# Optimization experiments

Measured on AMD Instinct MI355X. Metric: run time of the kernel, lower is better.

The kernel has to match this reference:

```python
import jax, jax.numpy as jnp
import numpy as np

B, N, T, FB, HID, NC = 1024, 64, 256, 5, 64, 3
T2 = T // 2
EPS = 1e-5


def setup_inputs() -> dict:
    key = jax.random.key(0)
    ks = jax.random.split(key, 40)
    it = iter(range(40))
    def nrm(shape, s=0.1):
        return (jax.random.normal(ks[next(it)], shape, dtype=jnp.float32) * s)
    inp = {}
    inp["x_T"] = jax.random.normal(ks[next(it)], (B, N, T), dtype=jnp.float32)
    inp["x_F"] = jax.random.normal(ks[next(it)], (B, N, FB), dtype=jnp.float32)
    inp["A"] = jax.random.uniform(ks[next(it)], (B, N, N), dtype=jnp.float32)
    # STDCN_F (seq len = FB, input=hidden=N)
    inp["gcnw_F"] = jnp.full((1, 1), 10.0, dtype=jnp.float32)
    for d in ("f", "b"):
        inp[f"gru_F_wih_{d}"] = nrm((3 * N, N))
        inp[f"gru_F_whh_{d}"] = nrm((3 * N, N))
        inp[f"gru_F_bih_{d}"] = nrm((3 * N,))
        inp[f"gru_F_bhh_{d}"] = nrm((3 * N,))
    inp["bn_F_g"] = jnp.ones((FB,), jnp.float32)
    inp["bn_F_b"] = jnp.zeros((FB,), jnp.float32)
    # STDCN_T (seq len = T)
    inp["gcnw_T"] = jnp.full((1, 1), 10.0, dtype=jnp.float32)
    for d in ("f", "b"):
        inp[f"gru_T_wih_{d}"] = nrm((3 * N, N))
        inp[f"gru_T_whh_{d}"] = nrm((3 * N, N))
        inp[f"gru_T_bih_{d}"] = nrm((3 * N,))
        inp[f"gru_T_bhh_{d}"] = nrm((3 * N,))
    inp["bn_T_g"] = jnp.ones((T,), jnp.float32)
    inp["bn_T_b"] = jnp.zeros((T,), jnp.float32)
    # heads
    inp["linF_w"] = nrm((T2, FB))
    inp["linF_b"] = nrm((T2,))
    inp["linT_w"] = nrm((T2, T), 0.05)
    inp["linT_b"] = nrm((T2,))
    inp["lin1_w"] = nrm((HID, T * N * 2), 0.01)
    inp["lin1_b"] = nrm((HID,))
    inp["lin2_w"] = nrm((NC, HID))
    inp["lin2_b"] = nrm((NC,))
    return inp


def _leaky(x):
    return jnp.where(x >= 0, x, 0.01 * x)


def _norm_adj(A):
    # zero diagonal, add self loops, symmetric D^-1/2 A D^-1/2
    I = jnp.eye(A.shape[1], dtype=A.dtype)
    H = A * (1.0 - I) + I
    dinv = jnp.sum(H, axis=-1) ** -0.5  # [B,N]
    return dinv[:, :, None] * H * dinv[:, None, :]


def _gru_dir(x, wih, whh, bih, bhh):
    # x: [B,S,N] -> outputs [B,S,Nh]; torch GRU cell equations
    gx = jnp.einsum("bsn,gn->bsg", x, wih) + bih  # [B,S,3Nh]
    gx = jnp.swapaxes(gx, 0, 1)  # [S,B,3Nh]
    Nh = whh.shape[1]
    h0 = jnp.zeros((x.shape[0], Nh), x.dtype)
    def step(h, g):
        gh = h @ whh.T + bhh
        xr, xz, xn = jnp.split(g, 3, axis=-1)
        hr, hz, hn = jnp.split(gh, 3, axis=-1)
        r = jax.nn.sigmoid(xr + hr)
        z = jax.nn.sigmoid(xz + hz)
        n = jnp.tanh(xn + r * hn)
        h = (1.0 - z) * n + z * h
        return h, h
    _, hs = jax.lax.scan(step, h0, gx)
    return jnp.swapaxes(hs, 0, 1)


def _gru_bi(x, pf, pb):
    f = _gru_dir(x, *pf)
    b = _gru_dir(x[:, ::-1], *pb)[:, ::-1]
    return jnp.concatenate([f, b], axis=-1)


def _batchnorm(x, g, b):
    # x: [B, F, C]; BatchNorm1d over channel dim 1, training-mode batch stats
    m = jnp.mean(x, axis=(0, 2), keepdims=True)
    v = jnp.var(x, axis=(0, 2), keepdims=True)
    return g[None, :, None] * (x - m) / jnp.sqrt(v + EPS) + b[None, :, None]


def _stdcn(X, Hn, w, pf, pb, g, bparam):
    # gcn_conv loop == (H @ X) * scalar weight
    Xc = _leaky(jnp.einsum("bij,bjf->bif", Hn, X) * w[0, 0])
    Xp = jnp.swapaxes(Xc, 1, 2)  # [B,F,N]
    o = _gru_bi(Xp, pf, pb)      # [B,F,2N]
    o = _batchnorm(o, g, bparam)
    return jnp.swapaxes(o, 1, 2)  # [B,2N,F]


def reference(x_T, x_F, A, gcnw_F, gru_F_wih_f, gru_F_whh_f, gru_F_bih_f, gru_F_bhh_f,
              gru_F_wih_b, gru_F_whh_b, gru_F_bih_b, gru_F_bhh_b, bn_F_g, bn_F_b,
              gcnw_T, gru_T_wih_f, gru_T_whh_f, gru_T_bih_f, gru_T_bhh_f,
              gru_T_wih_b, gru_T_whh_b, gru_T_bih_b, gru_T_bhh_b, bn_T_g, bn_T_b,
              linF_w, linF_b, linT_w, linT_b, lin1_w, lin1_b, lin2_w, lin2_b):
    Hn = _norm_adj(A)
    out_F = _stdcn(x_F, Hn, gcnw_F,
                   (gru_F_wih_f, gru_F_whh_f, gru_F_bih_f, gru_F_bhh_f),
                   (gru_F_wih_b, gru_F_whh_b, gru_F_bih_b, gru_F_bhh_b),
                   bn_F_g, bn_F_b)  # [B,2N,FB]
    out_F = (out_F @ linF_w.T + linF_b).reshape(out_F.shape[0], -1)  # [B, 2N*T2]
    out_T = _stdcn(x_T, Hn, gcnw_T,
                   (gru_T_wih_f, gru_T_whh_f, gru_T_bih_f, gru_T_bhh_f),
                   (gru_T_wih_b, gru_T_whh_b, gru_T_bih_b, gru_T_bhh_b),
                   bn_T_g, bn_T_b)  # [B,2N,T]
    out_T = (out_T @ linT_w.T + linT_b).reshape(out_T.shape[0], -1)
    out = jnp.concatenate([out_F, out_T], axis=-1)  # [B, 2*N*T]
    out = _leaky(out @ lin1_w.T + lin1_b)
    return out @ lin2_w.T + lin2_b  # [B, NC]
```

## Files before the change

kernel.cpp:

```cpp
#include <hip/hip_runtime.h>

#define B_ 1024
#define N_ 64
#define T_ 256
#define FB_ 5
#define T2_ 128
#define C_ 128

typedef unsigned short u16;
typedef __attribute__((ext_vector_type(8))) short bf16x8;
typedef __attribute__((ext_vector_type(4))) float f32x4;

__device__ __forceinline__ float leaky(float x) { return x >= 0.f ? x : 0.01f * x; }
__device__ __forceinline__ float rcpf(float x) { return __builtin_amdgcn_rcpf(x); }
__device__ __forceinline__ float sigm2(float x) { return rcpf(1.f + __expf(-x)); }
__device__ __forceinline__ float tanh2(float x) { return 1.f - 2.f * rcpf(1.f + __expf(2.f * x)); }
__device__ __forceinline__ unsigned bf16_rne(float f) {
  unsigned u = __float_as_uint(f);
  return (u + 0x7FFFu + ((u >> 16) & 1u)) >> 16;
}
__device__ __forceinline__ void block_sync_lds() {
  __builtin_amdgcn_sched_barrier(0);
  asm volatile("s_waitcnt lgkmcnt(0)" ::: "memory");
  __builtin_amdgcn_s_barrier();
  __builtin_amdgcn_sched_barrier(0);
}

#define MFMA_(A, B, C) __builtin_amdgcn_mfma_f32_16x16x32_bf16(A, B, C, 0, 0, 0)

__device__ __forceinline__ void xc_tile(const float (*HsT)[68], float (*xs)[68],
                                        const float* __restrict__ Xb, int S, int t0, float w,
                                        float* __restrict__ Ob, int tid) {
  __syncthreads();
  for (int idx = tid; idx < 4096; idx += 256) {
    int j = idx >> 6, tt = idx & 63;
    xs[j][tt] = (t0 + tt < S) ? Xb[j * S + t0 + tt] : 0.f;
  }
  __syncthreads();
  int i0 = (tid & 15) * 4, tl = (tid >> 4) * 4;
  f32x4 a0 = {0, 0, 0, 0}, a1 = {0, 0, 0, 0}, a2 = {0, 0, 0, 0}, a3 = {0, 0, 0, 0};
#pragma unroll 4
  for (int j = 0; j < 64; ++j) {
    f32x4 hv = *(const f32x4*)&HsT[j][i0];
    f32x4 xv = *(const f32x4*)&xs[j][tl];
    a0 += hv * xv[0];
    a1 += hv * xv[1];
    a2 += hv * xv[2];
    a3 += hv * xv[3];
  }
#define STORE_T(K, AV)                                  \
  {                                                     \
    int t = t0 + tl + K;                                \
    if (t < S) {                                        \
      f32x4 r;                                          \
      _Pragma("unroll") for (int e = 0; e < 4; ++e)     \
          r[e] = leaky(w * AV[e]);                      \
      *(f32x4*)&Ob[(size_t)t * 64 + i0] = r;            \
    }                                                   \
  }
  STORE_T(0, a0)
  STORE_T(1, a1)
  STORE_T(2, a2)
  STORE_T(3, a3)
#undef STORE_T
}

__global__ __launch_bounds__(256) void knorm_xc(
    const float* __restrict__ A, const float* __restrict__ xT, const float* __restrict__ xF,
    const float* __restrict__ wT, const float* __restrict__ wF,
    float* __restrict__ XpT, float* __restrict__ XpF) {
  __shared__ float HsT[64][68];
  __shared__ float dinv[64];
  __shared__ float xs[64][68];
  int b = blockIdx.x, tid = threadIdx.x;
  const float* Ab = A + (size_t)b * 4096;
  for (int idx = tid; idx < 4096; idx += 256) {
    int i = idx >> 6, j = idx & 63;
    HsT[j][i] = (i == j) ? 1.f : Ab[idx];
  }
  __syncthreads();
  if (tid < 64) {
    float s = 0.f;
    for (int j = 0; j < 64; ++j) s += HsT[j][tid];
    dinv[tid] = 1.f / sqrtf(s);
  }
  __syncthreads();
  for (int idx = tid; idx < 4096; idx += 256) {
    int j = idx >> 6, i = idx & 63;
    HsT[j][i] *= dinv[i] * dinv[j];
  }
  {
    const float* Xb = xT + (size_t)b * 64 * 256;
    float w = wT[0];
    float* Ob = XpT + (size_t)b * 256 * 64;
    for (int t0 = 0; t0 < 256; t0 += 64) xc_tile(HsT, xs, Xb, 256, t0, w, Ob, tid);
  }
  {
    const float* Xb = xF + (size_t)b * 64 * 5;
    float w = wF[0];
    float* Ob = XpF + (size_t)b * 5 * 64;
    xc_tile(HsT, xs, Xb, 5, 0, w, Ob, tid);
  }
}

__global__ __launch_bounds__(256) void kxq_all(const float* __restrict__ XpT,
                                               const float* __restrict__ XpF,
                                               u16* __restrict__ XfT, u16* __restrict__ XfF) {
  __shared__ float xs[4][16][68];
  int bt = blockIdx.x, by = blockIdx.y, tid = threadIdx.x;
  const float* Xp;
  u16* Xf;
  int S, t0;
  if (by < 64) {
    Xp = XpT; Xf = XfT; S = 256; t0 = by * 4;
  } else {
    Xp = XpF; Xf = XfF; S = 5; t0 = (by - 64) * 4;
  }
  for (int idx = tid; idx < 1024; idx += 256) {
    int b_l = idx >> 6, rest = idx & 63, t_l = rest >> 4, c = rest & 15;
    float4 v = {0.f, 0.f, 0.f, 0.f};
    if (t0 + t_l < S)
      v = *(const float4*)(Xp + ((size_t)(bt * 16 + b_l) * S + t0 + t_l) * 64 + c * 4);
    *(float4*)&xs[t_l][b_l][c * 4] = v;
  }
  __syncthreads();
  int t_l = tid >> 6, lane = tid & 63, blo = lane & 15, grp = lane >> 4;
  int t = t0 + t_l;
  if (t >= S) return;
#pragma unroll
  for (int kh = 0; kh < 2; ++kh) {
    const f32x4* src = (const f32x4*)&xs[t_l][blo][kh * 32 + grp * 8];
    f32x4 a0 = src[0], a1 = src[1];
    bf16x8 hi, lo;
#pragma unroll
    for (int e = 0; e < 4; ++e) {
      unsigned h0 = bf16_rne(a0[e]);
      hi[e] = (short)h0;
      lo[e] = (short)bf16_rne(a0[e] - __uint_as_float(h0 << 16));
      unsigned h1 = bf16_rne(a1[e]);
      hi[e + 4] = (short)h1;
      lo[e + 4] = (short)bf16_rne(a1[e] - __uint_as_float(h1 << 16));
    }
    u16* dst = Xf + (size_t)(bt * S + t) * 2048 + (size_t)kh * 1024 + lane * 8;
    *(bf16x8*)dst = hi;
    *(bf16x8*)(dst + 512) = lo;
  }
}

__device__ __forceinline__ void axcomp(f32x4 (&AX)[3], const bf16x8 (&XB)[4],
                                       const bf16x8 (&Whi)[3][2], const bf16x8 (&Wlo)[3][2],
                                       const f32x4 (&bI)[3]) {
  AX[0] = bI[0];
  AX[1] = bI[1];
  AX[2] = bI[2];
#pragma unroll
  for (int kh = 0; kh < 2; ++kh) {
    bf16x8 xh = XB[2 * kh], xl = XB[2 * kh + 1];
#pragma unroll
    for (int gi = 0; gi < 3; ++gi) {
      AX[gi] = MFMA_(Whi[gi][kh], xh, AX[gi]);
      AX[gi] = MFMA_(Whi[gi][kh], xl, AX[gi]);
      AX[gi] = MFMA_(Wlo[gi][kh], xh, AX[gi]);
    }
  }
}

__global__ __launch_bounds__(256, 1) void kgru_all(
    const u16* __restrict__ XfT, const u16* __restrict__ XfF,
    const float* __restrict__ Twih_f, const float* __restrict__ Twhh_f,
    const float* __restrict__ Tbih_f, const float* __restrict__ Tbhh_f,
    const float* __restrict__ Twih_b, const float* __restrict__ Twhh_b,
    const float* __restrict__ Tbih_b, const float* __restrict__ Tbhh_b,
    const float* __restrict__ Fwih_f, const float* __restrict__ Fwhh_f,
    const float* __restrict__ Fbih_f, const float* __restrict__ Fbhh_f,
    const float* __restrict__ Fwih_b, const float* __restrict__ Fwhh_b,
    const float* __restrict__ Fbih_b, const float* __restrict__ Fbhh_b,
    u16* __restrict__ gT, u16* __restrict__ gF,
    const float* __restrict__ W1, const float* __restrict__ lTw, const float* __restrict__ lFw,
    const float* __restrict__ lFb, const float* __restrict__ lTb, const float* __restrict__ l1b,
    float* __restrict__ MT, float* __restrict__ MF, float* __restrict__ c0v) {
  __shared__ u16 Hhi[2][16][72];
  __shared__ u16 Hlo[2][16][72];
  __shared__ float W1s[128][129];
  __shared__ float ls[128][32];
  __shared__ float rs[256];
  int tid = threadIdx.x;
  int w = tid >> 6, lane = tid & 63, blo = lane & 15, grp = lane >> 4;
  int bt = blockIdx.x, dir = blockIdx.y, tf = blockIdx.z;
  int S = tf ? 5 : 256;
  const u16* Xf = tf ? XfF : XfT;
  u16* g = tf ? gF : gT;
  const float* wih = tf ? (dir ? Fwih_b : Fwih_f) : (dir ? Twih_b : Twih_f);
  const float* whh = tf ? (dir ? Fwhh_b : Fwhh_f) : (dir ? Twhh_b : Twhh_f);
  const float* bih = tf ? (dir ? Fbih_b : Fbih_f) : (dir ? Tbih_b : Tbih_f);
  const float* bhh = tf ? (dir ? Fbhh_b : Fbhh_f) : (dir ? Tbhh_b : Tbhh_f);

  for (int idx = tid; idx < 16 * 72; idx += 256) {
    ((u16*)Hhi[0])[idx] = 0;
    ((u16*)Hlo[0])[idx] = 0;
  }

  bf16x8 Wih_hi[3][2], Wih_lo[3][2], Whh_hi[3][2], Whh_lo[3][2];
#pragma unroll
  for (int gi = 0; gi < 3; ++gi) {
    int k = (gi * 4 + w) * 16 + blo;
#pragma unroll
    for (int kh = 0; kh < 2; ++kh) {
      int j0 = kh * 32 + grp * 8;
#pragma unroll
      for (int m = 0; m < 2; ++m) {
        const float* src = (m ? whh : wih) + (size_t)k * 64 + j0;
        f32x4 a0 = *(const f32x4*)src;
        f32x4 a1 = *(const f32x4*)(src + 4);
        bf16x8 hi, lo;
#pragma unroll
        for (int e = 0; e < 4; ++e) {
          unsigned h0 = bf16_rne(a0[e]);
          hi[e] = (short)h0;
          lo[e] = (short)bf16_rne(a0[e] - __uint_as_float(h0 << 16));
          unsigned h1 = bf16_rne(a1[e]);
          hi[e + 4] = (short)h1;
          lo[e + 4] = (short)bf16_rne(a1[e] - __uint_as_float(h1 << 16));
        }
        if (m) {
          Whh_hi[gi][kh] = hi;
          Whh_lo[gi][kh] = lo;
        } else {
          Wih_hi[gi][kh] = hi;
          Wih_lo[gi][kh] = lo;
        }
      }
    }
  }
  f32x4 bI[3], bH[3];
#pragma unroll
  for (int gi = 0; gi < 3; ++gi) {
    int k0 = (gi * 4 + w) * 16 + 4 * grp;
    bI[gi] = *(const f32x4*)(bih + k0);
    bH[gi] = *(const f32x4*)(bhh + k0);
  }

  float ho[4] = {0.f, 0.f, 0.f, 0.f};
  int j0q = 16 * w + 4 * grp;
  const u16* xbase = Xf + (size_t)bt * S * 2048 + lane * 8;
  long long sstep = dir ? -4096LL : 4096LL;
  long long gstep = dir ? -256LL : 256LL;

  bf16x8 x0[4], x1[4], x2[4], x3[4];
#define LOADX(DST, TR)                            \
  {                                               \
    const u16* xp = xbase + (size_t)(TR) * 2048;  \
    DST[0] = *(const bf16x8*)(xp);                \
    DST[1] = *(const bf16x8*)(xp + 512);          \
    DST[2] = *(const bf16x8*)(xp + 1024);         \
    DST[3] = *(const bf16x8*)(xp + 1536);         \
  }
  LOADX(x0, dir ? (S - 1) : 0)
  if (S > 1) LOADX(x1, dir ? (S - 2) : 1)
  if (S > 2) LOADX(x2, dir ? (S - 3) : 2)
  const u16* xw = xbase + (size_t)(dir ? (S >= 4 ? S - 4 : 0) : 3) * 2048;
  u16* gp = g + ((size_t)(bt * 16 + blo) * S + (dir ? S - 1 : 0)) * 128 + dir * 64 + j0q;

  f32x4 axA[3], axB[3];
  axcomp(axA, x0, Wih_hi, Wih_lo, bI);
  block_sync_lds();

#define GSTEP(KK, XAX, XLD, AXC, AXN, PR, PW)                                        \
  {                                                                                  \
    int t = tbase + KK;                                                              \
    if (t < S) {                                                                     \
      bf16x8 h0h = *(const bf16x8*)&Hhi[PR][blo][grp * 8];                           \
      bf16x8 h0l = *(const bf16x8*)&Hlo[PR][blo][grp * 8];                           \
      bf16x8 h1h = *(const bf16x8*)&Hhi[PR][blo][32 + grp * 8];                      \
      bf16x8 h1l = *(const bf16x8*)&Hlo[PR][blo][32 + grp * 8];                      \
      if (t + 3 < S) {                                                               \
        XLD[0] = *(const bf16x8*)(xw);                                               \
        XLD[1] = *(const bf16x8*)(xw + 512);                                         \
        XLD[2] = *(const bf16x8*)(xw + 1024);                                        \
        XLD[3] = *(const bf16x8*)(xw + 1536);                                        \
        xw = (const u16*)((const char*)xw + sstep);                                  \
      }                                                                              \
      if (t + 1 < S) axcomp(AXN, XAX, Wih_hi, Wih_lo, bI);                           \
      f32x4 ahr = bH[0], ahz = bH[1], ahn = bH[2];                                   \
      ahr = MFMA_(Whh_hi[0][0], h0h, ahr);                                           \
      ahr = MFMA_(Whh_hi[0][0], h0l, ahr);                                           \
      ahr = MFMA_(Whh_lo[0][0], h0h, ahr);                                           \
      ahz = MFMA_(Whh_hi[1][0], h0h, ahz);                                           \
      ahz = MFMA_(Whh_hi[1][0], h0l, ahz);                                           \
      ahz = MFMA_(Whh_lo[1][0], h0h, ahz);                                           \
      ahn = MFMA_(Whh_hi[2][0], h0h, ahn);                                           \
      ahn = MFMA_(Whh_hi[2][0], h0l, ahn);                                           \
      ahn = MFMA_(Whh_lo[2][0], h0h, ahn);                                           \
      ahr = MFMA_(Whh_hi[0][1], h1h, ahr);                                           \
      ahr = MFMA_(Whh_hi[0][1], h1l, ahr);                                           \
      ahr = MFMA_(Whh_lo[0][1], h1h, ahr);                                           \
      ahz = MFMA_(Whh_hi[1][1], h1h, ahz);                                           \
      ahz = MFMA_(Whh_hi[1][1], h1l, ahz);                                           \
      ahz = MFMA_(Whh_lo[1][1], h1h, ahz);                                           \
      ahn = MFMA_(Whh_hi[2][1], h1h, ahn);                                           \
      ahn = MFMA_(Whh_hi[2][1], h1l, ahn);                                           \
      ahn = MFMA_(Whh_lo[2][1], h1h, ahn);                                           \
      u16 hi_u[4], lo_u[4];                                                          \
      _Pragma("unroll") for (int u = 0; u < 4; ++u) {                                \
        float r = sigm2(AXC[0][u] + ahr[u]);                                         \
        float z = sigm2(AXC[1][u] + ahz[u]);                                         \
        float n = tanh2(AXC[2][u] + r * ahn[u]);                                     \
        float h = n + z * (ho[u] - n);                                               \
        ho[u] = h;                                                                   \
        unsigned hb = (__float_as_uint(h) + 0x8000u) >> 16;                          \
        hi_u[u] = (u16)hb;                                                           \
        float rr = h - __uint_as_float(hb << 16);                                    \
        lo_u[u] = (u16)((__float_as_uint(rr) + 0x8000u) >> 16);                      \
      }                                                                              \
      ushort4 h4;                                                                    \
      h4.x = hi_u[0]; h4.y = hi_u[1]; h4.z = hi_u[2]; h4.w = hi_u[3];                \
      ushort4 l4;                                                                    \
      l4.x = lo_u[0]; l4.y = lo_u[1]; l4.z = lo_u[2]; l4.w = lo_u[3];                \
      *(ushort4*)&Hhi[PW][blo][j0q] = h4;                                            \
      *(ushort4*)&Hlo[PW][blo][j0q] = l4;                                            \
      *(ushort4*)gp = h4;                                                            \
      gp = (u16*)((char*)gp + gstep);                                                \
      block_sync_lds();                                                              \
    }                                                                                \
  }

  for (int tbase = 0; tbase < S; tbase += 4) {
    GSTEP(0, x1, x3, axA, axB, 0, 1)
    GSTEP(1, x2, x0, axB, axA, 1, 0)
    GSTEP(2, x3, x1, axA, axB, 0, 1)
    GSTEP(3, x0, x2, axB, axA, 1, 0)
  }
#undef GSTEP
#undef LOADX

  if (tf == 1) {
    int jid = bt * 2 + dir;
    for (int job = jid; job < 576; job += 128) {
      __syncthreads();
      int o = job & 63, by = job >> 6;
      if (by < 8) {
        int t0 = by * 32;
        const float* Wo = W1 + (size_t)o * 32768 + 16384;
        for (int idx = tid; idx < 16384; idx += 256) W1s[idx >> 7][idx & 127] = Wo[idx];
        for (int idx = tid; idx < 4096; idx += 256)
          ls[idx >> 5][idx & 31] = lTw[(idx >> 5) * 256 + t0 + (idx & 31)];
        __syncthreads();
        int c = tid & 127, th = tid >> 7;
        float acc[16];
#pragma unroll
        for (int q = 0; q < 16; ++q) acc[q] = 0.f;
        for (int t2 = 0; t2 < 128; ++t2) {
          float wv = W1s[c][t2];
#pragma unroll
          for (int q = 0; q < 16; ++q) acc[q] += wv * ls[t2][th + 2 * q];
        }
        float* Mo = MT + (size_t)o * 32768;
#pragma unroll
        for (int q = 0; q < 16; ++q) Mo[(t0 + th + 2 * q) * 128 + c] = acc[q];
      } else {
        const float* Wo = W1 + (size_t)o * 32768;
        for (int idx = tid; idx < 16384; idx += 256) W1s[idx >> 7][idx & 127] = Wo[idx];
        for (int idx = tid; idx < 640; idx += 256) ls[idx / 5][idx % 5] = lFw[idx];
        __syncthreads();
        int c = tid & 127, fh = tid >> 7;
        float acc[3] = {0.f, 0.f, 0.f};
        for (int t2 = 0; t2 < 128; ++t2) {
          float wv = W1s[c][t2];
#pragma unroll
          for (int q = 0; q < 3; ++q) {
            int f = fh + 2 * q;
            if (f < 5) acc[q] += wv * ls[t2][f];
          }
        }
#pragma unroll
        for (int q = 0; q < 3; ++q) {
          int f = fh + 2 * q;
          if (f < 5) MF[(size_t)o * 640 + f * 128 + c] = acc[q];
        }
        float s = 0.f;
        for (int idx = tid; idx < 16384; idx += 256) {
          int t2 = idx & 127;
          s += Wo[idx] * lFb[t2] + Wo[16384 + idx] * lTb[t2];
        }
        rs[tid] = s;
        __syncthreads();
        for (int off = 128; off; off >>= 1) {
          if (tid < off) rs[tid] += rs[tid + off];
          __syncthreads();
        }
        if (tid == 0) c0v[o] = l1b[o] + rs[0];
      }
    }
  }
}

__global__ __launch_bounds__(256) void kbn_all(
    const u16* __restrict__ gTp, const u16* __restrict__ gFp,
    const float* __restrict__ gamT, const float* __restrict__ betT,
    const float* __restrict__ gamF, const float* __restrict__ betF,
    float* __restrict__ sdT, float* __restrict__ sdF) {
  int bid = blockIdx.x, tid = threadIdx.x;
  const u16* g;
  const float *gam, *bet;
  float* sd;
  int S, t;
  if (bid < 256) {
    g = gTp; S = 256; t = bid; gam = gamT; bet = betT; sd = sdT;
  } else {
    g = gFp; S = 5; t = bid - 256; gam = gamF; bet = betF; sd = sdF;
  }
  float s = 0.f, s2 = 0.f;
  for (int unit = tid; unit < 32768; unit += 256) {
    int b = unit >> 5, c4 = (unit & 31) * 4;
    ushort4 u = *(const ushort4*)(g + ((size_t)b * S + t) * 128 + c4);
    float v0 = __uint_as_float((unsigned)u.x << 16);
    float v1 = __uint_as_float((unsigned)u.y << 16);
    float v2 = __uint_as_float((unsigned)u.z << 16);
    float v3 = __uint_as_float((unsigned)u.w << 16);
    s += v0 + v1 + v2 + v3;
    s2 += v0 * v0 + v1 * v1 + v2 * v2 + v3 * v3;
  }
  __shared__ float rs[256], rq[256];
  rs[tid] = s;
  rq[tid] = s2;
  __syncthreads();
  for (int off = 128; off; off >>= 1) {
    if (tid < off) {
      rs[tid] += rs[tid + off];
      rq[tid] += rq[tid + off];
    }
    __syncthreads();
  }
  if (tid == 0) {
    float inv_n = 1.f / (float)(B_ * C_);
    float m = rs[0] * inv_n;
    float var = rq[0] * inv_n - m * m;
    float inv = 1.f / sqrtf(var + 1e-5f);
    float sc = gam[t] * inv;
    sd[2 * t] = sc;
    sd[2 * t + 1] = bet[t] - m * sc;
  }
}

__global__ __launch_bounds__(256) void kchunk_all(
    const u16* __restrict__ gTp, const u16* __restrict__ gFp,
    const float* __restrict__ sdT, const float* __restrict__ sdF,
    const float* __restrict__ MT, const float* __restrict__ MF,
    float* __restrict__ part) {
  __shared__ float gs[32][132];
  __shared__ float Ms[64][132];
  int tid = threadIdx.x;
  int b0 = blockIdx.x * 32;
  int by = blockIdx.y;
  const u16* g;
  const float *sd, *M;
  int S, nt, t0, slot;
  if (by < 16) {
    g = gTp; sd = sdT; M = MT; S = 256; nt = 16; t0 = by * 16; slot = by;
  } else {
    g = gFp; sd = sdF; M = MF; S = 5; nt = 5; t0 = 0; slot = 16;
  }
  int ot = tid & 31, bt = tid >> 5;
  float acc[4][2];
#pragma unroll
  for (int i = 0; i < 4; ++i) {
    acc[i][0] = 0.f;
    acc[i][1] = 0.f;
  }
  for (int t = t0; t < t0 + nt; ++t) {
    __syncthreads();
    float sc = sd[2 * t], dd = sd[2 * t + 1];
    for (int idx = tid; idx < 1024; idx += 256) {
      int bb = idx >> 5, c4 = (idx & 31) * 4;
      ushort4 u = *(const ushort4*)(g + ((size_t)(b0 + bb) * S + t) * 128 + c4);
      gs[bb][c4 + 0] = __uint_as_float((unsigned)u.x << 16) * sc + dd;
      gs[bb][c4 + 1] = __uint_as_float((unsigned)u.y << 16) * sc + dd;
      gs[bb][c4 + 2] = __uint_as_float((unsigned)u.z << 16) * sc + dd;
      gs[bb][c4 + 3] = __uint_as_float((unsigned)u.w << 16) * sc + dd;
    }
    for (int idx = tid; idx < 2048; idx += 256) {
      int o = idx >> 5, c4 = (idx & 31) * 4;
      *(float4*)&Ms[o][c4] = *(const float4*)(M + ((size_t)o * S + t) * 128 + c4);
    }
    __syncthreads();
    for (int c = 0; c < 128; c += 4) {
      f32x4 m0 = *(const f32x4*)&Ms[ot][c];
      f32x4 m1 = *(const f32x4*)&Ms[ot + 32][c];
#pragma unroll
      for (int i = 0; i < 4; ++i) {
        f32x4 gv = *(const f32x4*)&gs[bt * 4 + i][c];
        acc[i][0] += gv[0] * m0[0] + gv[1] * m0[1] + gv[2] * m0[2] + gv[3] * m0[3];
        acc[i][1] += gv[0] * m1[0] + gv[1] * m1[1] + gv[2] * m1[2] + gv[3] * m1[3];
      }
    }
  }
#pragma unroll
  for (int i = 0; i < 4; ++i) {
    part[((size_t)slot * 1024 + b0 + bt * 4 + i) * 64 + ot] = acc[i][0];
    part[((size_t)slot * 1024 + b0 + bt * 4 + i) * 64 + ot + 32] = acc[i][1];
  }
}

__global__ __launch_bounds__(64) void kfin(const float* __restrict__ part,
                                           const float* __restrict__ c0,
                                           const float* __restrict__ l2w,
                                           const float* __restrict__ l2b,
                                           float* __restrict__ outp) {
  int b = blockIdx.x, o = threadIdx.x;
  float y = c0[o];
  for (int s = 0; s < 17; ++s) y += part[((size_t)s * 1024 + b) * 64 + o];
  y = leaky(y);
  __shared__ float a[64];
  a[o] = y;
  __syncthreads();
  if (o < 3) {
    float r = l2b[o];
    for (int j = 0; j < 64; ++j) r += l2w[o * 64 + j] * a[j];
    outp[b * 3 + o] = r;
  }
}

extern "C" void kernel_launch(void* const* d_in, const int* in_sizes, int n_in,
                              void* d_out, int out_size, void* d_ws, size_t ws_size,
                              hipStream_t stream) {
  const float* x_T = (const float*)d_in[0];
  const float* x_F = (const float*)d_in[1];
  const float* A = (const float*)d_in[2];
  const float* gcnw_F = (const float*)d_in[3];
  const float* gFwih_f = (const float*)d_in[4];
  const float* gFwhh_f = (const float*)d_in[5];
  const float* gFbih_f = (const float*)d_in[6];
  const float* gFbhh_f = (const float*)d_in[7];
  const float* gFwih_b = (const float*)d_in[8];
  const float* gFwhh_b = (const float*)d_in[9];
  const float* gFbih_b = (const float*)d_in[10];
  const float* gFbhh_b = (const float*)d_in[11];
  const float* bnFg = (const float*)d_in[12];
  const float* bnFb = (const float*)d_in[13];
  const float* gcnw_T = (const float*)d_in[14];
  const float* gTwih_f = (const float*)d_in[15];
  const float* gTwhh_f = (const float*)d_in[16];
  const float* gTbih_f = (const float*)d_in[17];
  const float* gTbhh_f = (const float*)d_in[18];
  const float* gTwih_b = (const float*)d_in[19];
  const float* gTwhh_b = (const float*)d_in[20];
  const float* gTbih_b = (const float*)d_in[21];
  const float* gTbhh_b = (const float*)d_in[22];
  const float* bnTg = (const float*)d_in[23];
  const float* bnTb = (const float*)d_in[24];
  const float* linF_w = (const float*)d_in[25];
  const float* linF_b = (const float*)d_in[26];
  const float* linT_w = (const float*)d_in[27];
  const float* linT_b = (const float*)d_in[28];
  const float* lin1_w = (const float*)d_in[29];
  const float* lin1_b = (const float*)d_in[30];
  const float* lin2_w = (const float*)d_in[31];
  const float* lin2_b = (const float*)d_in[32];

  char* w8 = (char*)d_ws;
  size_t off = 0;
  auto take = [&](size_t bytes) {
    void* p = w8 + off;
    off += (bytes + 255) & ~(size_t)255;
    return p;
  };
  float* XpT = (float*)take((size_t)1024 * 256 * 64 * 4);
  float* XpF = (float*)take((size_t)1024 * 5 * 64 * 4);
  u16* XfT = (u16*)take((size_t)64 * 256 * 2048 * 2);
  u16* XfF = (u16*)take((size_t)64 * 5 * 2048 * 2);
  u16* gT = (u16*)take((size_t)1024 * 256 * 128 * 2);
  u16* gF = (u16*)take((size_t)1024 * 5 * 128 * 2);
  float* sdT = (float*)take(512 * 4);
  float* sdF = (float*)take(16 * 4);
  float* MT = (float*)take((size_t)64 * 256 * 128 * 4);
  float* MF = (float*)take((size_t)64 * 5 * 128 * 4);
  float* c0 = (float*)take(64 * 4);
  float* part = (float*)take((size_t)17 * 1024 * 64 * 4);

  knorm_xc<<<1024, 256, 0, stream>>>(A, x_T, x_F, gcnw_T, gcnw_F, XpT, XpF);
  kxq_all<<<dim3(64, 66), 256, 0, stream>>>(XpT, XpF, XfT, XfF);
  kgru_all<<<dim3(64, 2, 2), 256, 0, stream>>>(
      XfT, XfF, gTwih_f, gTwhh_f, gTbih_f, gTbhh_f, gTwih_b, gTwhh_b, gTbih_b, gTbhh_b,
      gFwih_f, gFwhh_f, gFbih_f, gFbhh_f, gFwih_b, gFwhh_b, gFbih_b, gFbhh_b, gT, gF,
      lin1_w, linT_w, linF_w, linF_b, linT_b, lin1_b, MT, MF, c0);
  kbn_all<<<261, 256, 0, stream>>>(gT, gF, bnTg, bnTb, bnFg, bnFb, sdT, sdF);
  kchunk_all<<<dim3(32, 17), 256, 0, stream>>>(gT, gF, sdT, sdF, MT, MF, part);
  kfin<<<1024, 64, 0, stream>>>(part, c0, lin2_w, lin2_b, (float*)d_out);
}
```

Before: 484.3 us.

## Split GRU hidden-dim reduction across two wave groups with LDS partial sums

Doubles the GRU block to 512 threads and splits the 64-wide K dimension of each gate matmul between two groups of four waves. The second group writes partial gate sums to shared memory, and the first group combines them and applies the nonlinearity. This halves the serial MFMA chain per timestep on the recurrent critical path. In exchange it adds an extra barrier and LDS round-trip per step, and it rescales the epilogue W1-projection work to 512 threads.

```diff
diff --git a/kernel.cpp b/kernel.cpp
--- a/kernel.cpp
+++ b/kernel.cpp
@@ -147,25 +147,21 @@
   }
 }
 
-__device__ __forceinline__ void axcomp(f32x4 (&AX)[3], const bf16x8 (&XB)[4],
-                                       const bf16x8 (&Whi)[3][2], const bf16x8 (&Wlo)[3][2],
-                                       const f32x4 (&bI)[3]) {
-  AX[0] = bI[0];
-  AX[1] = bI[1];
-  AX[2] = bI[2];
-#pragma unroll
-  for (int kh = 0; kh < 2; ++kh) {
-    bf16x8 xh = XB[2 * kh], xl = XB[2 * kh + 1];
-#pragma unroll
-    for (int gi = 0; gi < 3; ++gi) {
-      AX[gi] = MFMA_(Whi[gi][kh], xh, AX[gi]);
-      AX[gi] = MFMA_(Whi[gi][kh], xl, AX[gi]);
-      AX[gi] = MFMA_(Wlo[gi][kh], xh, AX[gi]);
-    }
-  }
-}
-
-__global__ __launch_bounds__(256, 1) void kgru_all(
+__device__ __forceinline__ void axc_h(f32x4 (&AX)[3], const bf16x8 (&XB)[2],
+                                      const bf16x8 (&Whi)[3], const bf16x8 (&Wlo)[3],
+                                      const f32x4 (&bI)[3]) {
+  bf16x8 xh = XB[0], xl = XB[1];
+#pragma unroll
+  for (int gi = 0; gi < 3; ++gi) {
+    f32x4 a = bI[gi];
+    a = MFMA_(Whi[gi], xh, a);
+    a = MFMA_(Whi[gi], xl, a);
+    a = MFMA_(Wlo[gi], xh, a);
+    AX[gi] = a;
+  }
+}
+
+__global__ __launch_bounds__(512, 1) void kgru_all(
     const u16* __restrict__ XfT, const u16* __restrict__ XfF,
     const float* __restrict__ Twih_f, const float* __restrict__ Twhh_f,
     const float* __restrict__ Tbih_f, const float* __restrict__ Tbhh_f,
@@ -181,11 +177,13 @@
     float* __restrict__ MT, float* __restrict__ MF, float* __restrict__ c0v) {
   __shared__ u16 Hhi[2][16][72];
   __shared__ u16 Hlo[2][16][72];
+  __shared__ float PS[4][4][16][20];
   __shared__ float W1s[128][129];
   __shared__ float ls[128][32];
-  __shared__ float rs[256];
+  __shared__ float rs[512];
   int tid = threadIdx.x;
-  int w = tid >> 6, lane = tid & 63, blo = lane & 15, grp = lane >> 4;
+  int wave = tid >> 6, lane = tid & 63, blo = lane & 15, grp = lane >> 4;
+  int w = wave & 3, kh = wave >> 2;
   int bt = blockIdx.x, dir = blockIdx.y, tf = blockIdx.z;
   int S = tf ? 5 : 256;
   const u16* Xf = tf ? XfF : XfT;
@@ -195,65 +193,66 @@
   const float* bih = tf ? (dir ? Fbih_b : Fbih_f) : (dir ? Tbih_b : Tbih_f);
   const float* bhh = tf ? (dir ? Fbhh_b : Fbhh_f) : (dir ? Tbhh_b : Tbhh_f);
 
-  for (int idx = tid; idx < 16 * 72; idx += 256) {
+  for (int idx = tid; idx < 16 * 72; idx += 512) {
     ((u16*)Hhi[0])[idx] = 0;
     ((u16*)Hlo[0])[idx] = 0;
   }
 
-  bf16x8 Wih_hi[3][2], Wih_lo[3][2], Whh_hi[3][2], Whh_lo[3][2];
+  bf16x8 Wih_hi[3], Wih_lo[3], Whh_hi[3], Whh_lo[3];
 #pragma unroll
   for (int gi = 0; gi < 3; ++gi) {
     int k = (gi * 4 + w) * 16 + blo;
-#pragma unroll
-    for (int kh = 0; kh < 2; ++kh) {
-      int j0 = kh * 32 + grp * 8;
-#pragma unroll
-      for (int m = 0; m < 2; ++m) {
-        const float* src = (m ? whh : wih) + (size_t)k * 64 + j0;
-        f32x4 a0 = *(const f32x4*)src;
-        f32x4 a1 = *(const f32x4*)(src + 4);
-        bf16x8 hi, lo;
-#pragma unroll
-        for (int e = 0; e < 4; ++e) {
-          unsigned h0 = bf16_rne(a0[e]);
-          hi[e] = (short)h0;
-          lo[e] = (short)bf16_rne(a0[e] - __uint_as_float(h0 << 16));
-          unsigned h1 = bf16_rne(a1[e]);
-          hi[e + 4] = (short)h1;
-          lo[e + 4] = (short)bf16_rne(a1[e] - __uint_as_float(h1 << 16));
-        }
-        if (m) {
-          Whh_hi[gi][kh] = hi;
-          Whh_lo[gi][kh] = lo;
-        } else {
-          Wih_hi[gi][kh] = hi;
-          Wih_lo[gi][kh] = lo;
-        }
+    int j0 = kh * 32 + grp * 8;
+#pragma unroll
+    for (int m = 0; m < 2; ++m) {
+      const float* src = (m ? whh : wih) + (size_t)k * 64 + j0;
+      f32x4 a0 = *(const f32x4*)src;
+      f32x4 a1 = *(const f32x4*)(src + 4);
+      bf16x8 hi, lo;
+#pragma unroll
+      for (int e = 0; e < 4; ++e) {
+        unsigned h0 = bf16_rne(a0[e]);
+        hi[e] = (short)h0;
+        lo[e] = (short)bf16_rne(a0[e] - __uint_as_float(h0 << 16));
+        unsigned h1 = bf16_rne(a1[e]);
+        hi[e + 4] = (short)h1;
+        lo[e + 4] = (short)bf16_rne(a1[e] - __uint_as_float(h1 << 16));
       }
+      if (m) {
+        Whh_hi[gi] = hi;
+        Whh_lo[gi] = lo;
+      } else {
+        Wih_hi[gi] = hi;
+        Wih_lo[gi] = lo;
+      }
     }
   }
   f32x4 bI[3], bH[3];
 #pragma unroll
   for (int gi = 0; gi < 3; ++gi) {
-    int k0 = (gi * 4 + w) * 16 + 4 * grp;
-    bI[gi] = *(const f32x4*)(bih + k0);
-    bH[gi] = *(const f32x4*)(bhh + k0);
+    if (kh == 0) {
+      int k0 = (gi * 4 + w) * 16 + 4 * grp;
+      bI[gi] = *(const f32x4*)(bih + k0);
+      bH[gi] = *(const f32x4*)(bhh + k0);
+    } else {
+      bI[gi] = (f32x4){0.f, 0.f, 0.f, 0.f};
+      bH[gi] = (f32x4){0.f, 0.f, 0.f, 0.f};
+    }
   }
 
   float ho[4] = {0.f, 0.f, 0.f, 0.f};
   int j0q = 16 * w + 4 * grp;
-  const u16* xbase = Xf + (size_t)bt * S * 2048 + lane * 8;
+  int grp4 = grp * 4, kh32 = kh * 32;
+  const u16* xbase = Xf + (size_t)bt * S * 2048 + (size_t)kh * 1024 + lane * 8;
   long long sstep = dir ? -4096LL : 4096LL;
   long long gstep = dir ? -256LL : 256LL;
 
-  bf16x8 x0[4], x1[4], x2[4], x3[4];
+  bf16x8 x0[2], x1[2], x2[2], x3[2];
 #define LOADX(DST, TR)                            \
   {                                               \
     const u16* xp = xbase + (size_t)(TR) * 2048;  \
     DST[0] = *(const bf16x8*)(xp);                \
     DST[1] = *(const bf16x8*)(xp + 512);          \
-    DST[2] = *(const bf16x8*)(xp + 1024);         \
-    DST[3] = *(const bf16x8*)(xp + 1536);         \
   }
   LOADX(x0, dir ? (S - 1) : 0)
   if (S > 1) LOADX(x1, dir ? (S - 2) : 1)
@@ -262,64 +261,64 @@
   u16* gp = g + ((size_t)(bt * 16 + blo) * S + (dir ? S - 1 : 0)) * 128 + dir * 64 + j0q;
 
   f32x4 axA[3], axB[3];
-  axcomp(axA, x0, Wih_hi, Wih_lo, bI);
+  axc_h(axA, x0, Wih_hi, Wih_lo, bI);
   block_sync_lds();
 
 #define GSTEP(KK, XAX, XLD, AXC, AXN, PR, PW)                                        \
   {                                                                                  \
     int t = tbase + KK;                                                              \
     if (t < S) {                                                                     \
-      bf16x8 h0h = *(const bf16x8*)&Hhi[PR][blo][grp * 8];                           \
-      bf16x8 h0l = *(const bf16x8*)&Hlo[PR][blo][grp * 8];                           \
-      bf16x8 h1h = *(const bf16x8*)&Hhi[PR][blo][32 + grp * 8];                      \
-      bf16x8 h1l = *(const bf16x8*)&Hlo[PR][blo][32 + grp * 8];                      \
+      bf16x8 hh = *(const bf16x8*)&Hhi[PR][blo][kh32 + grp * 8];                     \
+      bf16x8 hl = *(const bf16x8*)&Hlo[PR][blo][kh32 + grp * 8];                     \
       if (t + 3 < S) {                                                               \
         XLD[0] = *(const bf16x8*)(xw);                                               \
         XLD[1] = *(const bf16x8*)(xw + 512);                                         \
-        XLD[2] = *(const bf16x8*)(xw + 1024);                                        \
-        XLD[3] = *(const bf16x8*)(xw + 1536);                                        \
         xw = (const u16*)((const char*)xw + sstep);                                  \
       }                                                                              \
-      if (t + 1 < S) axcomp(AXN, XAX, Wih_hi, Wih_lo, bI);                           \
       f32x4 ahr = bH[0], ahz = bH[1], ahn = bH[2];                                   \
-      ahr = MFMA_(Whh_hi[0][0], h0h, ahr);                                           \
-      ahr = MFMA_(Whh_hi[0][0], h0l, ahr);                                           \
-      ahr = MFMA_(Whh_lo[0][0], h0h, ahr);                                           \
-      ahz = MFMA_(Whh_hi[1][0], h0h, ahz);                                           \
-      ahz = MFMA_(Whh_hi[1][0], h0l, ahz);                                           \
-      ahz = MFMA_(Whh_lo[1][0], h0h, ahz);                                           \
-      ahn = MFMA_(Whh_hi[2][0], h0h, ahn);                                           \
-      ahn = MFMA_(Whh_hi[2][0], h0l, ahn);                                           \
-      ahn = MFMA_(Whh_lo[2][0], h0h, ahn);                                           \
-      ahr = MFMA_(Whh_hi[0][1], h1h, ahr);                                           \
-      ahr = MFMA_(Whh_hi[0][1], h1l, ahr);                                           \
-      ahr = MFMA_(Whh_lo[0][1], h1h, ahr);                                           \
-      ahz = MFMA_(Whh_hi[1][1], h1h, ahz);                                           \
-      ahz = MFMA_(Whh_hi[1][1], h1l, ahz);                                           \
-      ahz = MFMA_(Whh_lo[1][1], h1h, ahz);                                           \
-      ahn = MFMA_(Whh_hi[2][1], h1h, ahn);                                           \
-      ahn = MFMA_(Whh_hi[2][1], h1l, ahn);                                           \
-      ahn = MFMA_(Whh_lo[2][1], h1h, ahn);                                           \
-      u16 hi_u[4], lo_u[4];                                                          \
-      _Pragma("unroll") for (int u = 0; u < 4; ++u) {                                \
-        float r = sigm2(AXC[0][u] + ahr[u]);                                         \
-        float z = sigm2(AXC[1][u] + ahz[u]);                                         \
-        float n = tanh2(AXC[2][u] + r * ahn[u]);                                     \
-        float h = n + z * (ho[u] - n);                                               \
-        ho[u] = h;                                                                   \
-        unsigned hb = (__float_as_uint(h) + 0x8000u) >> 16;                          \
-        hi_u[u] = (u16)hb;                                                           \
-        float rr = h - __uint_as_float(hb << 16);                                    \
-        lo_u[u] = (u16)((__float_as_uint(rr) + 0x8000u) >> 16);                      \
+      ahr = MFMA_(Whh_hi[0], hh, ahr);                                               \
+      ahr = MFMA_(Whh_hi[0], hl, ahr);                                               \
+      ahr = MFMA_(Whh_lo[0], hh, ahr);                                               \
+      ahz = MFMA_(Whh_hi[1], hh, ahz);                                               \
+      ahz = MFMA_(Whh_hi[1], hl, ahz);                                               \
+      ahz = MFMA_(Whh_lo[1], hh, ahz);                                               \
+      ahn = MFMA_(Whh_hi[2], hh, ahn);                                               \
+      ahn = MFMA_(Whh_hi[2], hl, ahn);                                               \
+      ahn = MFMA_(Whh_lo[2], hh, ahn);                                               \
+      if (t + 1 < S) axc_h(AXN, XAX, Wih_hi, Wih_lo, bI);                            \
+      if (kh) {                                                                      \
+        *(f32x4*)&PS[0][w][blo][grp4] = ahr + AXC[0];                                \
+        *(f32x4*)&PS[1][w][blo][grp4] = ahz + AXC[1];                                \
+        *(f32x4*)&PS[2][w][blo][grp4] = ahn;                                         \
+        *(f32x4*)&PS[3][w][blo][grp4] = AXC[2];                                      \
       }                                                                              \
-      ushort4 h4;                                                                    \
-      h4.x = hi_u[0]; h4.y = hi_u[1]; h4.z = hi_u[2]; h4.w = hi_u[3];                \
-      ushort4 l4;                                                                    \
-      l4.x = lo_u[0]; l4.y = lo_u[1]; l4.z = lo_u[2]; l4.w = lo_u[3];                \
-      *(ushort4*)&Hhi[PW][blo][j0q] = h4;                                            \
-      *(ushort4*)&Hlo[PW][blo][j0q] = l4;                                            \
-      *(ushort4*)gp = h4;                                                            \
-      gp = (u16*)((char*)gp + gstep);                                                \
+      block_sync_lds();                                                              \
+      if (!kh) {                                                                     \
+        f32x4 pr = *(const f32x4*)&PS[0][w][blo][grp4];                              \
+        f32x4 pz = *(const f32x4*)&PS[1][w][blo][grp4];                              \
+        f32x4 pan = *(const f32x4*)&PS[2][w][blo][grp4];                             \
+        f32x4 pxn = *(const f32x4*)&PS[3][w][blo][grp4];                             \
+        u16 hi_u[4], lo_u[4];                                                        \
+        _Pragma("unroll") for (int u = 0; u < 4; ++u) {                              \
+          float r = sigm2(AXC[0][u] + ahr[u] + pr[u]);                               \
+          float z = sigm2(AXC[1][u] + ahz[u] + pz[u]);                               \
+          float n = tanh2((AXC[2][u] + pxn[u]) + r * (ahn[u] + pan[u]));             \
+          float h = n + z * (ho[u] - n);                                             \
+          ho[u] = h;                                                                 \
+          unsigned hb = (__float_as_uint(h) + 0x8000u) >> 16;                        \
+          hi_u[u] = (u16)hb;                                                         \
+          float rr = h - __uint_as_float(hb << 16);                                  \
+          lo_u[u] = (u16)((__float_as_uint(rr) + 0x8000u) >> 16);                    \
+        }                                                                            \
+        ushort4 h4;                                                                  \
+        h4.x = hi_u[0]; h4.y = hi_u[1]; h4.z = hi_u[2]; h4.w = hi_u[3];              \
+        ushort4 l4;                                                                  \
+        l4.x = lo_u[0]; l4.y = lo_u[1]; l4.z = lo_u[2]; l4.w = lo_u[3];              \
+        *(ushort4*)&Hhi[PW][blo][j0q] = h4;                                          \
+        *(ushort4*)&Hlo[PW][blo][j0q] = l4;                                          \
+        *(ushort4*)gp = h4;                                                          \
+        gp = (u16*)((char*)gp + gstep);                                              \
+      }                                                                              \
       block_sync_lds();                                                              \
     }                                                                                \
   }
@@ -337,54 +336,54 @@
     int jid = bt * 2 + dir;
     for (int job = jid; job < 576; job += 128) {
       __syncthreads();
-      int o = job & 63, by = job >> 6;
-      if (by < 8) {
-        int t0 = by * 32;
+      int o = job & 63, byy = job >> 6;
+      if (byy < 8) {
+        int t0 = byy * 32;
         const float* Wo = W1 + (size_t)o * 32768 + 16384;
-        for (int idx = tid; idx < 16384; idx += 256) W1s[idx >> 7][idx & 127] = Wo[idx];
-        for (int idx = tid; idx < 4096; idx += 256)
+        for (int idx = tid; idx < 16384; idx += 512) W1s[idx >> 7][idx & 127] = Wo[idx];
+        for (int idx = tid; idx < 4096; idx += 512)
           ls[idx >> 5][idx & 31] = lTw[(idx >> 5) * 256 + t0 + (idx & 31)];
         __syncthreads();
         int c = tid & 127, th = tid >> 7;
-        float acc[16];
-#pragma unroll
-        for (int q = 0; q < 16; ++q) acc[q] = 0.f;
+        float acc[8];
+#pragma unroll
+        for (int q = 0; q < 8; ++q) acc[q] = 0.f;
         for (int t2 = 0; t2 < 128; ++t2) {
           float wv = W1s[c][t2];
 #pragma unroll
-          for (int q = 0; q < 16; ++q) acc[q] += wv * ls[t2][th + 2 * q];
+          for (int q = 0; q < 8; ++q) acc[q] += wv * ls[t2][th + 4 * q];
         }
         float* Mo = MT + (size_t)o * 32768;
 #pragma unroll
-        for (int q = 0; q < 16; ++q) Mo[(t0 + th + 2 * q) * 128 + c] = acc[q];
+        for (int q = 0; q < 8; ++q) Mo[(t0 + th + 4 * q) * 128 + c] = acc[q];
       } else {
         const float* Wo = W1 + (size_t)o * 32768;
-        for (int idx = tid; idx < 16384; idx += 256) W1s[idx >> 7][idx & 127] = Wo[idx];
-        for (int idx = tid; idx < 640; idx += 256) ls[idx / 5][idx % 5] = lFw[idx];
+        for (int idx = tid; idx < 16384; idx += 512) W1s[idx >> 7][idx & 127] = Wo[idx];
+        for (int idx = tid; idx < 640; idx += 512) ls[idx / 5][idx % 5] = lFw[idx];
         __syncthreads();
         int c = tid & 127, fh = tid >> 7;
-        float acc[3] = {0.f, 0.f, 0.f};
+        float acc[2] = {0.f, 0.f};
         for (int t2 = 0; t2 < 128; ++t2) {
           float wv = W1s[c][t2];
 #pragma unroll
-          for (int q = 0; q < 3; ++q) {
-            int f = fh + 2 * q;
+          for (int q = 0; q < 2; ++q) {
+            int f = fh + 4 * q;
             if (f < 5) acc[q] += wv * ls[t2][f];
           }
         }
 #pragma unroll
-        for (int q = 0; q < 3; ++q) {
-          int f = fh + 2 * q;
+        for (int q = 0; q < 2; ++q) {
+          int f = fh + 4 * q;
           if (f < 5) MF[(size_t)o * 640 + f * 128 + c] = acc[q];
         }
         float s = 0.f;
-        for (int idx = tid; idx < 16384; idx += 256) {
+        for (int idx = tid; idx < 16384; idx += 512) {
           int t2 = idx & 127;
           s += Wo[idx] * lFb[t2] + Wo[16384 + idx] * lTb[t2];
         }
         rs[tid] = s;
         __syncthreads();
-        for (int off = 128; off; off >>= 1) {
+        for (int off = 256; off; off >>= 1) {
           if (tid < off) rs[tid] += rs[tid + off];
           __syncthreads();
         }
@@ -579,7 +578,7 @@
 
   knorm_xc<<<1024, 256, 0, stream>>>(A, x_T, x_F, gcnw_T, gcnw_F, XpT, XpF);
   kxq_all<<<dim3(64, 66), 256, 0, stream>>>(XpT, XpF, XfT, XfF);
-  kgru_all<<<dim3(64, 2, 2), 256, 0, stream>>>(
+  kgru_all<<<dim3(64, 2, 2), 512, 0, stream>>>(
       XfT, XfF, gTwih_f, gTwhh_f, gTbih_f, gTbhh_f, gTwih_b, gTwhh_b, gTbih_b, gTbhh_b,
       gFwih_f, gFwhh_f, gFbih_f, gFbhh_f, gFwih_b, gFwhh_b, gFbih_b, gFbhh_b, gT, gF,
       lin1_w, linT_w, linF_w, linF_b, linT_b, lin1_b, MT, MF, c0);
```

After: 495.9 us. 1.02x slower.

## Fuse bf16 hi/lo split into graph-conv kernel and relayout GRU input

Applied to the files above, without the earlier changes.

The graph-convolution kernel now stages its leaky-activated output in shared memory and writes the bf16 hi/lo split directly to the GRU input buffer, removing the separate quantisation kernel and the fp32 intermediate round trip through global memory. The GRU input layout changes to a per-batch contiguous 128-element block (hi and lo interleaved by k-half), so the GRU loads use small offsets within one row instead of strides of 512 elements. This cuts one launch and about 67 MB of global traffic, at the cost of an extra shared buffer and barrier per tile in the fused kernel.

```diff
diff --git a/kernel.cpp b/kernel.cpp
--- a/kernel.cpp
+++ b/kernel.cpp
@@ -28,9 +28,9 @@
 
 #define MFMA_(A, B, C) __builtin_amdgcn_mfma_f32_16x16x32_bf16(A, B, C, 0, 0, 0)
 
-__device__ __forceinline__ void xc_tile(const float (*HsT)[68], float (*xs)[68],
+__device__ __forceinline__ void xc_tile(const float (*HsT)[68], float (*xs)[68], float (*ys)[68],
                                         const float* __restrict__ Xb, int S, int t0, float w,
-                                        float* __restrict__ Ob, int tid) {
+                                        u16* __restrict__ Xft, int tid) {
   __syncthreads();
   for (int idx = tid; idx < 4096; idx += 256) {
     int j = idx >> 6, tt = idx & 63;
@@ -48,31 +48,54 @@
     a2 += hv * xv[2];
     a3 += hv * xv[3];
   }
-#define STORE_T(K, AV)                                  \
+#define YS_T(K, AV)                                     \
   {                                                     \
-    int t = t0 + tl + K;                                \
-    if (t < S) {                                        \
-      f32x4 r;                                          \
-      _Pragma("unroll") for (int e = 0; e < 4; ++e)     \
-          r[e] = leaky(w * AV[e]);                      \
-      *(f32x4*)&Ob[(size_t)t * 64 + i0] = r;            \
-    }                                                   \
-  }
-  STORE_T(0, a0)
-  STORE_T(1, a1)
-  STORE_T(2, a2)
-  STORE_T(3, a3)
-#undef STORE_T
+    f32x4 r;                                            \
+    _Pragma("unroll") for (int e = 0; e < 4; ++e)       \
+        r[e] = leaky(w * AV[e]);                        \
+    *(f32x4*)&ys[tl + K][i0] = r;                       \
+  }
+  YS_T(0, a0)
+  YS_T(1, a1)
+  YS_T(2, a2)
+  YS_T(3, a3)
+#undef YS_T
+  __syncthreads();
+  int t_l = tid >> 2, p = tid & 3;
+  if (t0 + t_l < S) {
+    const f32x4* yr = (const f32x4*)&ys[t_l][p * 16];
+    f32x4 y0 = yr[0], y1 = yr[1], y2 = yr[2], y3 = yr[3];
+    bf16x8 hiA, hiB, loA, loB;
+#pragma unroll
+    for (int e = 0; e < 4; ++e) {
+      unsigned h;
+      h = bf16_rne(y0[e]); hiA[e] = (short)h;
+      loA[e] = (short)bf16_rne(y0[e] - __uint_as_float(h << 16));
+      h = bf16_rne(y1[e]); hiA[4 + e] = (short)h;
+      loA[4 + e] = (short)bf16_rne(y1[e] - __uint_as_float(h << 16));
+      h = bf16_rne(y2[e]); hiB[e] = (short)h;
+      loB[e] = (short)bf16_rne(y2[e] - __uint_as_float(h << 16));
+      h = bf16_rne(y3[e]); hiB[4 + e] = (short)h;
+      loB[4 + e] = (short)bf16_rne(y3[e] - __uint_as_float(h << 16));
+    }
+    u16* dst = Xft + (size_t)(t0 + t_l) * 2048 + (p >> 1) * 64 + (p & 1) * 16;
+    *(bf16x8*)dst = hiA;
+    *(bf16x8*)(dst + 8) = hiB;
+    *(bf16x8*)(dst + 32) = loA;
+    *(bf16x8*)(dst + 40) = loB;
+  }
 }
 
 __global__ __launch_bounds__(256) void knorm_xc(
     const float* __restrict__ A, const float* __restrict__ xT, const float* __restrict__ xF,
     const float* __restrict__ wT, const float* __restrict__ wF,
-    float* __restrict__ XpT, float* __restrict__ XpF) {
+    u16* __restrict__ XfT, u16* __restrict__ XfF) {
   __shared__ float HsT[64][68];
   __shared__ float dinv[64];
   __shared__ float xs[64][68];
+  __shared__ float ys[64][68];
   int b = blockIdx.x, tid = threadIdx.x;
+  int bt = b >> 4, blo = b & 15;
   const float* Ab = A + (size_t)b * 4096;
   for (int idx = tid; idx < 4096; idx += 256) {
     int i = idx >> 6, j = idx & 63;
@@ -92,58 +115,14 @@
   {
     const float* Xb = xT + (size_t)b * 64 * 256;
     float w = wT[0];
-    float* Ob = XpT + (size_t)b * 256 * 64;
-    for (int t0 = 0; t0 < 256; t0 += 64) xc_tile(HsT, xs, Xb, 256, t0, w, Ob, tid);
+    u16* Xft = XfT + (size_t)bt * 256 * 2048 + blo * 128;
+    for (int t0 = 0; t0 < 256; t0 += 64) xc_tile(HsT, xs, ys, Xb, 256, t0, w, Xft, tid);
   }
   {
     const float* Xb = xF + (size_t)b * 64 * 5;
     float w = wF[0];
-    float* Ob = XpF + (size_t)b * 5 * 64;
-    xc_tile(HsT, xs, Xb, 5, 0, w, Ob, tid);
-  }
-}
-
-__global__ __launch_bounds__(256) void kxq_all(const float* __restrict__ XpT,
-                                               const float* __restrict__ XpF,
-                                               u16* __restrict__ XfT, u16* __restrict__ XfF) {
-  __shared__ float xs[4][16][68];
-  int bt = blockIdx.x, by = blockIdx.y, tid = threadIdx.x;
-  const float* Xp;
-  u16* Xf;
-  int S, t0;
-  if (by < 64) {
-    Xp = XpT; Xf = XfT; S = 256; t0 = by * 4;
-  } else {
-    Xp = XpF; Xf = XfF; S = 5; t0 = (by - 64) * 4;
-  }
-  for (int idx = tid; idx < 1024; idx += 256) {
-    int b_l = idx >> 6, rest = idx & 63, t_l = rest >> 4, c = rest & 15;
-    float4 v = {0.f, 0.f, 0.f, 0.f};
-    if (t0 + t_l < S)
-      v = *(const float4*)(Xp + ((size_t)(bt * 16 + b_l) * S + t0 + t_l) * 64 + c * 4);
-    *(float4*)&xs[t_l][b_l][c * 4] = v;
-  }
-  __syncthreads();
-  int t_l = tid >> 6, lane = tid & 63, blo = lane & 15, grp = lane >> 4;
-  int t = t0 + t_l;
-  if (t >= S) return;
-#pragma unroll
-  for (int kh = 0; kh < 2; ++kh) {
-    const f32x4* src = (const f32x4*)&xs[t_l][blo][kh * 32 + grp * 8];
-    f32x4 a0 = src[0], a1 = src[1];
-    bf16x8 hi, lo;
-#pragma unroll
-    for (int e = 0; e < 4; ++e) {
-      unsigned h0 = bf16_rne(a0[e]);
-      hi[e] = (short)h0;
-      lo[e] = (short)bf16_rne(a0[e] - __uint_as_float(h0 << 16));
-      unsigned h1 = bf16_rne(a1[e]);
-      hi[e + 4] = (short)h1;
-      lo[e + 4] = (short)bf16_rne(a1[e] - __uint_as_float(h1 << 16));
-    }
-    u16* dst = Xf + (size_t)(bt * S + t) * 2048 + (size_t)kh * 1024 + lane * 8;
-    *(bf16x8*)dst = hi;
-    *(bf16x8*)(dst + 512) = lo;
+    u16* Xft = XfF + (size_t)bt * 5 * 2048 + blo * 128;
+    xc_tile(HsT, xs, ys, Xb, 5, 0, w, Xft, tid);
   }
 }
 
@@ -242,7 +221,7 @@
 
   float ho[4] = {0.f, 0.f, 0.f, 0.f};
   int j0q = 16 * w + 4 * grp;
-  const u16* xbase = Xf + (size_t)bt * S * 2048 + lane * 8;
+  const u16* xbase = Xf + (size_t)bt * S * 2048 + blo * 128 + grp * 8;
   long long sstep = dir ? -4096LL : 4096LL;
   long long gstep = dir ? -256LL : 256LL;
 
@@ -251,9 +230,9 @@
   {                                               \
     const u16* xp = xbase + (size_t)(TR) * 2048;  \
     DST[0] = *(const bf16x8*)(xp);                \
-    DST[1] = *(const bf16x8*)(xp + 512);          \
-    DST[2] = *(const bf16x8*)(xp + 1024);         \
-    DST[3] = *(const bf16x8*)(xp + 1536);         \
+    DST[1] = *(const bf16x8*)(xp + 32);           \
+    DST[2] = *(const bf16x8*)(xp + 64);           \
+    DST[3] = *(const bf16x8*)(xp + 96);           \
   }
   LOADX(x0, dir ? (S - 1) : 0)
   if (S > 1) LOADX(x1, dir ? (S - 2) : 1)
@@ -275,9 +254,9 @@
       bf16x8 h1l = *(const bf16x8*)&Hlo[PR][blo][32 + grp * 8];                      \
       if (t + 3 < S) {                                                               \
         XLD[0] = *(const bf16x8*)(xw);                                               \
-        XLD[1] = *(const bf16x8*)(xw + 512);                                         \
-        XLD[2] = *(const bf16x8*)(xw + 1024);                                        \
-        XLD[3] = *(const bf16x8*)(xw + 1536);                                        \
+        XLD[1] = *(const bf16x8*)(xw + 32);                                          \
+        XLD[2] = *(const bf16x8*)(xw + 64);                                          \
+        XLD[3] = *(const bf16x8*)(xw + 96);                                          \
         xw = (const u16*)((const char*)xw + sstep);                                  \
       }                                                                              \
       if (t + 1 < S) axcomp(AXN, XAX, Wih_hi, Wih_lo, bI);                           \
@@ -564,8 +543,6 @@
     off += (bytes + 255) & ~(size_t)255;
     return p;
   };
-  float* XpT = (float*)take((size_t)1024 * 256 * 64 * 4);
-  float* XpF = (float*)take((size_t)1024 * 5 * 64 * 4);
   u16* XfT = (u16*)take((size_t)64 * 256 * 2048 * 2);
   u16* XfF = (u16*)take((size_t)64 * 5 * 2048 * 2);
   u16* gT = (u16*)take((size_t)1024 * 256 * 128 * 2);
@@ -577,8 +554,7 @@
   float* c0 = (float*)take(64 * 4);
   float* part = (float*)take((size_t)17 * 1024 * 64 * 4);
 
-  knorm_xc<<<1024, 256, 0, stream>>>(A, x_T, x_F, gcnw_T, gcnw_F, XpT, XpF);
-  kxq_all<<<dim3(64, 66), 256, 0, stream>>>(XpT, XpF, XfT, XfF);
+  knorm_xc<<<1024, 256, 0, stream>>>(A, x_T, x_F, gcnw_T, gcnw_F, XfT, XfF);
   kgru_all<<<dim3(64, 2, 2), 256, 0, stream>>>(
       XfT, XfF, gTwih_f, gTwhh_f, gTbih_f, gTbhh_f, gTwih_b, gTwhh_b, gTbih_b, gTbhh_b,
       gFwih_f, gFwhh_f, gFbih_f, gFbhh_f, gFwih_b, gFwhh_b, gFbih_b, gFbhh_b, gT, gF,
```

After: 530.9 us. 9.6% more time.
